# Performance work log

Hardware: AMD Instinct MI355X
Metric: run time of the kernel (lower is better)

Reference implementation:

```python
import jax, jax.numpy as jnp
import numpy as np

N_NODES = 100000
N_GRAPHS = 64


def gcn_conv(x, src, dst, W, b, num_nodes):
    """PyG GCNConv: add self-loops, symmetric deg normalization, aggregate at dst."""
    h = x @ W  # [N, out]
    ones_e = jnp.ones(src.shape[0], dtype=x.dtype)
    # degree includes self-loop (+1)
    deg = jax.ops.segment_sum(ones_e, dst, num_segments=num_nodes) + 1.0
    dinv = jnp.where(deg > 0, 1.0 / jnp.sqrt(deg), 0.0)  # deg>=1 always here
    norm = dinv[src] * dinv[dst]  # [E]
    msg = h[src] * norm[:, None]  # gather + scale
    agg = jax.ops.segment_sum(msg, dst, num_segments=num_nodes)
    # self-loop contribution: norm_ii = dinv[i]^2
    agg = agg + h * (dinv * dinv)[:, None]
    return agg + b


def global_mean_pool(x, batch, num_graphs):
    sums = jax.ops.segment_sum(x, batch, num_segments=num_graphs)
    counts = jax.ops.segment_sum(jnp.ones(x.shape[0], dtype=x.dtype), batch,
                                 num_segments=num_graphs)
    return sums / jnp.maximum(counts, 1.0)[:, None]


def setup_inputs() -> dict:
    key = jax.random.key(0)
    ks = jax.random.split(key, 8)
    H = 128
    x = jax.random.normal(ks[0], (N_NODES, 4), dtype=jnp.float32)
    edge_index = jax.random.randint(ks[1], (2, 1600000), 0, N_NODES, dtype=jnp.int64 if jax.config.read('jax_enable_x64') else jnp.int32)
    batch = jnp.sort(jax.random.randint(ks[2], (N_NODES,), 0, N_GRAPHS))
    def glorot(k, shape):
        fan_in, fan_out = shape
        lim = np.sqrt(6.0 / (fan_in + fan_out))
        return jax.random.uniform(k, shape, jnp.float32, -lim, lim)
    return {
        'x': x,
        'edge_index': edge_index,
        'batch': batch,
        'W1': glorot(ks[3], (4, H)), 'b1': jnp.zeros((H,), jnp.float32),
        'W2': glorot(ks[4], (H, H)), 'b2': jnp.zeros((H,), jnp.float32),
        'W3': glorot(ks[5], (H, H)), 'b3': jnp.zeros((H,), jnp.float32),
        'Wl': glorot(ks[6], (H, 2)), 'bl': jnp.zeros((2,), jnp.float32),
    }


def reference(x, edge_index, batch, W1, b1, W2, b2, W3, b3, Wl, bl):
    src, dst = edge_index[0], edge_index[1]
    h = jax.nn.relu(gcn_conv(x, src, dst, W1, b1, N_NODES))
    h = jax.nn.relu(gcn_conv(h, src, dst, W2, b2, N_NODES))
    h = jax.nn.relu(gcn_conv(h, src, dst, W3, b3, N_NODES))
    g = global_mean_pool(h, batch, N_GRAPHS)  # [G, H]
    logits = g @ Wl + bl  # [G, 2]
    return jax.nn.log_softmax(logits, axis=1)
```

## Files before the change

### kernel.cpp

```cpp
#include <hip/hip_runtime.h>

#define HDIM 128
#define NGRAPH 64

#define BSHIFT 9
#define NBUCK 196
#define BCAP 48
#define BSTR 49
#define RCAP 9216
#define BIN_CHUNK 4096

typedef __attribute__((ext_vector_type(8))) short short8;
typedef __attribute__((ext_vector_type(4))) float floatx4;
typedef __attribute__((ext_vector_type(2))) float floatx2;

__device__ __forceinline__ float bf2f(unsigned short u) {
    union { unsigned int i; float f; } v;
    v.i = ((unsigned int)u) << 16;
    return v.f;
}
__device__ __forceinline__ unsigned short f2bf(float f) {
    unsigned int u = __float_as_uint(f);
    u += 0x7FFFu + ((u >> 16) & 1u);
    return (unsigned short)(u >> 16);
}

__global__ __launch_bounds__(256) void k_misc(int* __restrict__ gcur,
                                              const int* __restrict__ batch,
                                              float* __restrict__ gcnt,
                                              float* __restrict__ gsum,
                                              const float* __restrict__ W2,
                                              unsigned short* __restrict__ Wp2,
                                              const float* __restrict__ W3,
                                              unsigned short* __restrict__ Wp3,
                                              int N, int nbuck) {
    int t = threadIdx.x;
    int blk = blockIdx.x;
    if (blk == 0) {
        if (t < nbuck) gcur[t] = t * RCAP;
        for (int i = t; i < NGRAPH * 128; i += 256) gsum[i] = 0.f;
        if (t < NGRAPH) {
            int g = t;
            int lo = 0, hi = N;
            while (lo < hi) { int m = (lo + hi) >> 1; if (batch[m] < g) lo = m + 1; else hi = m; }
            int lb = lo;
            lo = 0; hi = N;
            while (lo < hi) { int m = (lo + hi) >> 1; if (batch[m] < g + 1) lo = m + 1; else hi = m; }
            gcnt[g] = (float)(lo - lb);
        }
        return;
    }
    const float* W = (blk <= 64) ? W2 : W3;
    unsigned short* Wp = (blk <= 64) ? Wp2 : Wp3;
    int idx = ((blk <= 64) ? (blk - 1) : (blk - 65)) * 256 + t;
    int j = idx & 7, l = (idx >> 3) & 63, frag = idx >> 9;
    int c = frag >> 2, ks = frag & 3;
    int k = ks * 32 + ((l >> 4) & 3) * 8 + j;
    int n = c * 16 + (l & 15);
    Wp[idx] = f2bf(W[k * 128 + n]);
}


__global__ __launch_bounds__(256) void k_binA(const int* __restrict__ src,
                                              const int* __restrict__ dst,
                                              int* __restrict__ gcur,
                                              unsigned int* __restrict__ binned, int E) {
    __shared__ unsigned int bin[NBUCK * BSTR];
    __shared__ int bcnt[NBUCK];
    __shared__ int bbase[NBUCK];
    int t = threadIdx.x;
    for (int b = t; b < NBUCK; b += 256) bcnt[b] = 0;
    __syncthreads();
    int e0 = blockIdx.x * BIN_CHUNK;
    #pragma unroll
    for (int i = 0; i < BIN_CHUNK / 1024; i++) {
        int e = e0 + i * 1024 + t * 4;
        if (e + 3 < E) {
            const int4 d4 = *(const int4*)&dst[e];
            const int4 s4 = *(const int4*)&src[e];
            int dd[4] = {d4.x, d4.y, d4.z, d4.w};
            int ss[4] = {s4.x, s4.y, s4.z, s4.w};
            #pragma unroll
            for (int k = 0; k < 4; k++) {
                int d = dd[k];
                unsigned int rec = ((unsigned int)(d & 511) << 20) | (unsigned int)ss[k];
                int b = d >> BSHIFT;
                int idx = atomicAdd(&bcnt[b], 1);
                if (idx < BCAP) bin[b * BSTR + idx] = rec;
                else { int p = atomicAdd(&gcur[b], 1); binned[p] = rec; }
            }
        } else {
            for (int k = 0; k < 4; k++) {
                int e2 = e + k;
                if (e2 < E) {
                    int d = dst[e2];
                    unsigned int rec = ((unsigned int)(d & 511) << 20) | (unsigned int)src[e2];
                    int b = d >> BSHIFT;
                    int idx = atomicAdd(&bcnt[b], 1);
                    if (idx < BCAP) bin[b * BSTR + idx] = rec;
                    else { int p = atomicAdd(&gcur[b], 1); binned[p] = rec; }
                }
            }
        }
    }
    __syncthreads();
    if (t < NBUCK) {
        int cnt = min(bcnt[t], BCAP);
        bbase[t] = atomicAdd(&gcur[t], cnt);
    }
    __syncthreads();
    int wave = t >> 6, lane = t & 63;
    for (int b = wave; b < NBUCK; b += 4) {
        int cnt = min(bcnt[b], BCAP);
        int base = bbase[b];
        if (lane < cnt) binned[base + lane] = bin[b * BSTR + lane];
    }
}

__global__ __launch_bounds__(256) void k_fillB(const int* __restrict__ gcur,
                                               const unsigned int* __restrict__ binned,
                                               int* __restrict__ P,
                                               float* __restrict__ dinv,
                                               int* __restrict__ csr,
                                               const float4* __restrict__ x4,
                                               float4* __restrict__ xs4,
                                               int N, int nbuck) {
    __shared__ int ps[256];
    __shared__ int cnt[512];
    __shared__ int image[RCAP];
    int b = blockIdx.x;
    int t = threadIdx.x;
    int lt = (t < nbuck) ? (gcur[t] - t * RCAP) : 0;
    ps[t] = lt;
    __syncthreads();
    for (int d = 1; d < 256; d <<= 1) {
        int o = (t >= d) ? ps[t - d] : 0;
        __syncthreads();
        ps[t] += o;
        __syncthreads();
    }
    int start = (b > 0) ? ps[b - 1] : 0;
    int len = ps[b] - start;
    __syncthreads();

    int n0 = b << BSHIFT;
    int nloc = min(n0 + 512, N) - n0;
    cnt[t] = 0; cnt[t + 256] = 0;
    __syncthreads();
    const unsigned int* rb = binned + (size_t)b * RCAP;
    for (int i = t; i < len; i += 256) atomicAdd(&cnt[rb[i] >> 20], 1);
    __syncthreads();
    int c0 = cnt[2 * t], c1 = cnt[2 * t + 1];
    int pair = c0 + c1;
    __syncthreads();
    cnt[t] = pair;
    __syncthreads();
    for (int d = 1; d < 256; d <<= 1) {
        int o = (t >= d) ? cnt[t - d] : 0;
        __syncthreads();
        cnt[t] += o;
        __syncthreads();
    }
    int excl = cnt[t] - pair;
    __syncthreads();
    if (2 * t < nloc) {
        int n = n0 + 2 * t;
        float dv0 = rsqrtf((float)c0 + 1.0f);
        P[n] = start + excl;
        dinv[n] = dv0;
        float4 xv = x4[n];
        xs4[n] = make_float4(xv.x * dv0, xv.y * dv0, xv.z * dv0, xv.w * dv0);
    }
    if (2 * t + 1 < nloc) {
        int n = n0 + 2 * t + 1;
        float dv1 = rsqrtf((float)c1 + 1.0f);
        P[n] = start + excl + c0;
        dinv[n] = dv1;
        float4 xv = x4[n];
        xs4[n] = make_float4(xv.x * dv1, xv.y * dv1, xv.z * dv1, xv.w * dv1);
    }
    if (b == nbuck - 1 && t == 0) P[N] = start + len;
    cnt[2 * t] = excl;
    cnt[2 * t + 1] = excl + c0;
    __syncthreads();
    for (int i = t; i < len; i += 256) {
        unsigned int rec = rb[i];
        int pos = atomicAdd(&cnt[rec >> 20], 1);
        image[pos] = (int)(rec & 0xFFFFFu);
    }
    __syncthreads();
    for (int i = t; i < len; i += 256) csr[start + i] = image[i];
}

__global__ void k_aggx_csr(const int* __restrict__ P, const int* __restrict__ csr,
                           const float4* __restrict__ xs, const float* __restrict__ dinv,
                           float4* __restrict__ aggx, int N) {
    int d = blockIdx.x * blockDim.x + threadIdx.x;
    if (d >= N) return;
    int s0 = P[d], s1 = P[d + 1];
    float dd = dinv[d];
    float4 sv = xs[d];
    float4 a = make_float4(sv.x * dd, sv.y * dd, sv.z * dd, sv.w * dd);
    int i = s0;
    int pre = min(s1, (s0 + 3) & ~3);
    for (; i < pre; i++) {
        float4 v = xs[csr[i]];
        a.x += v.x; a.y += v.y; a.z += v.z; a.w += v.w;
    }
    for (; i + 8 <= s1; i += 8) {
        const int4 iA = *(const int4*)&csr[i];
        const int4 iB = *(const int4*)&csr[i + 4];
        float4 vA = xs[iA.x], vB = xs[iA.y], vC = xs[iA.z], vD = xs[iA.w];
        float4 vE = xs[iB.x], vF = xs[iB.y], vG = xs[iB.z], vH = xs[iB.w];
        a.x += vA.x + vB.x + vC.x + vD.x + vE.x + vF.x + vG.x + vH.x;
        a.y += vA.y + vB.y + vC.y + vD.y + vE.y + vF.y + vG.y + vH.y;
        a.z += vA.z + vB.z + vC.z + vD.z + vE.z + vF.z + vG.z + vH.z;
        a.w += vA.w + vB.w + vC.w + vD.w + vE.w + vF.w + vG.w + vH.w;
    }
    for (; i + 4 <= s1; i += 4) {
        const int4 ix = *(const int4*)&csr[i];
        float4 vA = xs[ix.x], vB = xs[ix.y], vC = xs[ix.z], vD = xs[ix.w];
        a.x += vA.x + vB.x + vC.x + vD.x;
        a.y += vA.y + vB.y + vC.y + vD.y;
        a.z += vA.z + vB.z + vC.z + vD.z;
        a.w += vA.w + vB.w + vC.w + vD.w;
    }
    for (; i < s1; i++) {
        float4 v = xs[csr[i]];
        a.x += v.x; a.y += v.y; a.z += v.z; a.w += v.w;
    }
    aggx[d] = make_float4(a.x * dd, a.y * dd, a.z * dd, a.w * dd);
}

#define LXS 136
__global__ __launch_bounds__(256) void k_l1t2(const float4* __restrict__ aggx,
                                              const float* __restrict__ W1,
                                              const float* __restrict__ b1,
                                              const unsigned short* __restrict__ Wp,
                                              const float* __restrict__ dinv,
                                              unsigned char* __restrict__ out8, int N) {
    __shared__ unsigned short lx[64 * LXS];
    __shared__ unsigned short lw[16384];
    __shared__ float w1s[512];
    __shared__ float b1s[128];
    __shared__ float ax[64][4];
    int t = threadIdx.x;
    int n0 = blockIdx.x * 64;

    for (int i = t; i < 512; i += 256) w1s[i] = W1[i];
    if (t < 128) b1s[t] = b1[t];
    if (t < 64) {
        float4 v = (n0 + t < N) ? aggx[n0 + t] : make_float4(0.f, 0.f, 0.f, 0.f);
        ax[t][0] = v.x; ax[t][1] = v.y; ax[t][2] = v.z; ax[t][3] = v.w;
    }
    for (int ch = t; ch < 2048; ch += 256)
        *(uint4*)&lw[ch * 8] = *(const uint4*)&Wp[ch * 8];
    __syncthreads();

    for (int i = t; i < 8192; i += 256) {
        int n = i >> 7, j = i & 127;
        float v = b1s[j] + ax[n][0] * w1s[j] + ax[n][1] * w1s[128 + j]
                         + ax[n][2] * w1s[256 + j] + ax[n][3] * w1s[384 + j];
        lx[n * LXS + j] = f2bf(fmaxf(v, 0.f));
    }
    __syncthreads();

    int w = t >> 6, lane = t & 63;
    int m0 = w * 16;
    int col = lane & 15, quad = lane >> 4;

    short8 afrag[4];
    #pragma unroll
    for (int ks = 0; ks < 4; ks++)
        afrag[ks] = *(const short8*)&lx[(m0 + col) * LXS + ks * 32 + quad * 8];

    float dv[4];
    #pragma unroll
    for (int r = 0; r < 4; r++) {
        int gn = n0 + m0 + quad * 4 + r;
        dv[r] = (gn < N) ? dinv[gn] : 0.0f;
    }

    #pragma unroll
    for (int c = 0; c < 8; c++) {
        floatx4 acc = {0.f, 0.f, 0.f, 0.f};
        #pragma unroll
        for (int ks = 0; ks < 4; ks++) {
            const short8 bfrag = *(const short8*)&lw[((c * 4 + ks) * 64 + lane) * 8];
            acc = __builtin_amdgcn_mfma_f32_16x16x32_bf16(afrag[ks], bfrag, acc, 0, 0, 0);
        }
        int j = c * 16 + col;
        size_t sbase = (size_t)(j >> 5) * N * 32 + (size_t)(j & 31);
        #pragma unroll
        for (int r = 0; r < 4; r++) {
            int gn = n0 + m0 + quad * 4 + r;
            if (gn < N) {
                float v = acc[r] * dv[r];
                out8[sbase + (size_t)gn * 32] =
                    (unsigned char)(__builtin_amdgcn_cvt_pk_fp8_f32(v, v, 0, false) & 0xFF);
            }
        }
    }
}

__global__ __launch_bounds__(256) void k_transform_mfma(const unsigned short* __restrict__ in,
                                                        const unsigned short* __restrict__ Wp,
                                                        const float* __restrict__ dinv,
                                                        unsigned char* __restrict__ out8, int N) {
    __shared__ unsigned short lx[64 * LXS];
    __shared__ unsigned short lw[16384];
    int t = threadIdx.x;
    int n0 = blockIdx.x * 64;

    for (int ch = t; ch < 1024; ch += 256) {
        int row = ch >> 4, part = ch & 15;
        uint4 val = make_uint4(0, 0, 0, 0);
        if (n0 + row < N) val = *(const uint4*)&in[(size_t)(n0 + row) * 128 + part * 8];
        *(uint4*)&lx[row * LXS + part * 8] = val;
    }
    for (int ch = t; ch < 2048; ch += 256)
        *(uint4*)&lw[ch * 8] = *(const uint4*)&Wp[ch * 8];
    __syncthreads();

    int w = t >> 6, lane = t & 63;
    int m0 = w * 16;
    int col = lane & 15, quad = lane >> 4;

    short8 afrag[4];
    #pragma unroll
    for (int ks = 0; ks < 4; ks++)
        afrag[ks] = *(const short8*)&lx[(m0 + col) * LXS + ks * 32 + quad * 8];

    float dv[4];
    #pragma unroll
    for (int r = 0; r < 4; r++) {
        int gn = n0 + m0 + quad * 4 + r;
        dv[r] = (gn < N) ? dinv[gn] : 0.0f;
    }

    #pragma unroll
    for (int c = 0; c < 8; c++) {
        floatx4 acc = {0.f, 0.f, 0.f, 0.f};
        #pragma unroll
        for (int ks = 0; ks < 4; ks++) {
            const short8 bfrag = *(const short8*)&lw[((c * 4 + ks) * 64 + lane) * 8];
            acc = __builtin_amdgcn_mfma_f32_16x16x32_bf16(afrag[ks], bfrag, acc, 0, 0, 0);
        }
        int j = c * 16 + col;
        size_t sbase = (size_t)(j >> 5) * N * 32 + (size_t)(j & 31);
        #pragma unroll
        for (int r = 0; r < 4; r++) {
            int gn = n0 + m0 + quad * 4 + r;
            if (gn < N) {
                float v = acc[r] * dv[r];
                out8[sbase + (size_t)gn * 32] =
                    (unsigned char)(__builtin_amdgcn_cvt_pk_fp8_f32(v, v, 0, false) & 0xFF);
            }
        }
    }
}

__device__ __forceinline__ void fp8acc(unsigned int u, float& a0, float& a1,
                                       float& a2, float& a3) {
    floatx2 lo = __builtin_amdgcn_cvt_pk_f32_fp8(u, false);
    floatx2 hi = __builtin_amdgcn_cvt_pk_f32_fp8(u, true);
    a0 += lo.x; a1 += lo.y; a2 += hi.x; a3 += hi.y;
}

__device__ __forceinline__ void gather8(const int* __restrict__ csr,
                                        const unsigned int* __restrict__ stab,
                                        int s0, int s1,
                                        float& a0, float& a1, float& a2, float& a3) {
    int i = s0;
    int pre = min(s1, (s0 + 3) & ~3);
    for (; i < pre; i++)
        fp8acc(stab[(size_t)csr[i] * 8], a0, a1, a2, a3);
    for (; i + 8 <= s1; i += 8) {
        const int4 iA = *(const int4*)&csr[i];
        const int4 iB = *(const int4*)&csr[i + 4];
        unsigned int u0 = stab[(size_t)iA.x * 8];
        unsigned int u1 = stab[(size_t)iA.y * 8];
        unsigned int u2 = stab[(size_t)iA.z * 8];
        unsigned int u3 = stab[(size_t)iA.w * 8];
        unsigned int u4 = stab[(size_t)iB.x * 8];
        unsigned int u5 = stab[(size_t)iB.y * 8];
        unsigned int u6 = stab[(size_t)iB.z * 8];
        unsigned int u7 = stab[(size_t)iB.w * 8];
        fp8acc(u0, a0, a1, a2, a3); fp8acc(u1, a0, a1, a2, a3);
        fp8acc(u2, a0, a1, a2, a3); fp8acc(u3, a0, a1, a2, a3);
        fp8acc(u4, a0, a1, a2, a3); fp8acc(u5, a0, a1, a2, a3);
        fp8acc(u6, a0, a1, a2, a3); fp8acc(u7, a0, a1, a2, a3);
    }
    for (; i + 4 <= s1; i += 4) {
        const int4 iA = *(const int4*)&csr[i];
        unsigned int u0 = stab[(size_t)iA.x * 8];
        unsigned int u1 = stab[(size_t)iA.y * 8];
        unsigned int u2 = stab[(size_t)iA.z * 8];
        unsigned int u3 = stab[(size_t)iA.w * 8];
        fp8acc(u0, a0, a1, a2, a3); fp8acc(u1, a0, a1, a2, a3);
        fp8acc(u2, a0, a1, a2, a3); fp8acc(u3, a0, a1, a2, a3);
    }
    for (; i < s1; i++)
        fp8acc(stab[(size_t)csr[i] * 8], a0, a1, a2, a3);
}

__global__ __launch_bounds__(256) void k_agg_sl(const int* __restrict__ P,
                                                const int* __restrict__ csr,
                                                const unsigned int* __restrict__ tab,
                                                const float* __restrict__ dinv,
                                                const float* __restrict__ bias,
                                                unsigned short* __restrict__ out16,
                                                const int* __restrict__ batch,
                                                float* __restrict__ gsum,
                                                int N, int mode) {
    __shared__ float psum[32][32];
    int t = threadIdx.x;
    int bid = blockIdx.x;
    int xcd = bid & 7;
    int slice = xcd >> 1;
    int chunk = (bid >> 3) * 2 + (xcd & 1);
    int nb = chunk * 32;
    int grp = t >> 3;
    int l = t & 7;
    int g = nb + grp;
    const unsigned int* stab = tab + (size_t)slice * N * 8 + l;

    float o0 = 0.f, o1 = 0.f, o2 = 0.f, o3 = 0.f;
    if (g < N) {
        int s0 = P[g], s1 = P[g + 1];
        unsigned int su = stab[(size_t)g * 8];
        floatx2 slo = __builtin_amdgcn_cvt_pk_f32_fp8(su, false);
        floatx2 shi = __builtin_amdgcn_cvt_pk_f32_fp8(su, true);
        float a0 = slo.x, a1 = slo.y, a2 = shi.x, a3 = shi.y;
        gather8(csr, stab, s0, s1, a0, a1, a2, a3);
        float dd = dinv[g];
        const float4 bb = *(const float4*)&bias[slice * 32 + l * 4];
        o0 = fmaxf(a0 * dd + bb.x, 0.f);
        o1 = fmaxf(a1 * dd + bb.y, 0.f);
        o2 = fmaxf(a2 * dd + bb.z, 0.f);
        o3 = fmaxf(a3 * dd + bb.w, 0.f);
        if (mode == 0) {
            ushort4 o;
            o.x = f2bf(o0); o.y = f2bf(o1); o.z = f2bf(o2); o.w = f2bf(o3);
            *(ushort4*)&out16[(size_t)g * 128 + slice * 32 + l * 4] = o;
        }
    }
    if (mode != 0) {
        *(float4*)&psum[grp][l * 4] = make_float4(o0, o1, o2, o3);
        __syncthreads();
        if (t < 32 && nb < N) {
            int f = t;
            int nbN = min(32, N - nb);
            int b0 = batch[nb], bL = batch[nb + nbN - 1];
            if (b0 == bL) {
                float s = 0.f;
                #pragma unroll
                for (int n = 0; n < 32; n++) s += psum[n][f];
                unsafeAtomicAdd(&gsum[(size_t)b0 * 128 + slice * 32 + f], s);
            } else {
                float acc = 0.f; int cur = b0;
                for (int n = 0; n < nbN; n++) {
                    int bb = batch[nb + n];
                    if (bb != cur) {
                        unsafeAtomicAdd(&gsum[(size_t)cur * 128 + slice * 32 + f], acc);
                        acc = 0.f; cur = bb;
                    }
                    acc += psum[n][f];
                }
                unsafeAtomicAdd(&gsum[(size_t)cur * 128 + slice * 32 + f], acc);
            }
        }
    }
}

__global__ __launch_bounds__(256) void k_head(const float* __restrict__ gsum,
                                              const float* __restrict__ gcnt,
                                              const float* __restrict__ Wl,
                                              const float* __restrict__ bl,
                                              float* __restrict__ out, int G) {
    int t = threadIdx.x;
    int g = t >> 2, q = t & 3;
    if (g >= G) return;
    float l0 = 0.f, l1 = 0.f;
    #pragma unroll
    for (int k = 0; k < 32; k++) {
        int jj = q * 32 + k;
        float v = gsum[(size_t)g * 128 + jj];
        l0 += v * Wl[jj * 2 + 0];
        l1 += v * Wl[jj * 2 + 1];
    }
    l0 += __shfl_xor(l0, 1, 64); l1 += __shfl_xor(l1, 1, 64);
    l0 += __shfl_xor(l0, 2, 64); l1 += __shfl_xor(l1, 2, 64);
    if (q == 0) {
        float inv = 1.0f / fmaxf(gcnt[g], 1.0f);
        l0 = l0 * inv + bl[0];
        l1 = l1 * inv + bl[1];
        float m = fmaxf(l0, l1);
        float lse = m + logf(expf(l0 - m) + expf(l1 - m));
        out[g * 2 + 0] = l0 - lse;
        out[g * 2 + 1] = l1 - lse;
    }
}


extern "C" void kernel_launch(void* const* d_in, const int* in_sizes, int n_in,
                              void* d_out, int out_size, void* d_ws, size_t ws_size,
                              hipStream_t stream) {
    const float* x   = (const float*)d_in[0];
    const int*   ei  = (const int*)d_in[1];
    const int*   bat = (const int*)d_in[2];
    const float* W1  = (const float*)d_in[3];
    const float* b1  = (const float*)d_in[4];
    const float* W2  = (const float*)d_in[5];
    const float* b2  = (const float*)d_in[6];
    const float* W3  = (const float*)d_in[7];
    const float* b3  = (const float*)d_in[8];
    const float* Wl  = (const float*)d_in[9];
    const float* bl  = (const float*)d_in[10];

    const int N = in_sizes[0] / 4;
    const int E = in_sizes[1] / 2;
    const int* srcI = ei;
    const int* dstI = ei + E;

    const int nbuck = (N + 511) >> BSHIFT;
    const int pAlloc = ((N + 1 + 3) & ~3) + 4;

    float* wsf  = (float*)d_ws;
    float* dinv = wsf;
    int*   P    = (int*)(dinv + N);
    int*   csr  = P + pAlloc;
    float* aggx = (float*)(csr + E);
    unsigned short* bufA16 = (unsigned short*)(aggx + (size_t)N * 4);
    unsigned char*  hs8    = (unsigned char*)(bufA16 + (size_t)N * 128);
    unsigned short* Wp2    = (unsigned short*)(hs8 + (size_t)N * 128);
    unsigned short* Wp3    = Wp2 + 16384;
    float* gsum = (float*)(Wp3 + 16384);
    float* gcnt = gsum + NGRAPH * 128;
    int*   gcur = (int*)(gcnt + NGRAPH);
    unsigned int* binned = (unsigned int*)hs8;
    float* xs4 = (float*)bufA16;

    const int chunks = (N + 31) >> 5;
    const int aggGrid = ((chunks + 1) >> 1) * 8;

    k_misc<<<129, 256, 0, stream>>>(gcur, bat, gcnt, gsum, W2, Wp2, W3, Wp3, N, nbuck);
    k_binA<<<(E + BIN_CHUNK - 1) / BIN_CHUNK, 256, 0, stream>>>(srcI, dstI, gcur, binned, E);
    k_fillB<<<nbuck, 256, 0, stream>>>(gcur, binned, P, dinv, csr,
                                       (const float4*)x, (float4*)xs4, N, nbuck);

    k_aggx_csr<<<(N + 255) / 256, 256, 0, stream>>>(P, csr, (const float4*)xs4, dinv,
                                                    (float4*)aggx, N);
    k_l1t2<<<(N + 63) / 64, 256, 0, stream>>>((const float4*)aggx, W1, b1, Wp2, dinv, hs8, N);

    k_agg_sl<<<aggGrid, 256, 0, stream>>>(P, csr, (const unsigned int*)hs8,
                                          dinv, b2, bufA16, nullptr, nullptr, N, 0);

    k_transform_mfma<<<(N + 63) / 64, 256, 0, stream>>>(bufA16, Wp3, dinv, hs8, N);
    k_agg_sl<<<aggGrid, 256, 0, stream>>>(P, csr, (const unsigned int*)hs8,
                                          dinv, b3, nullptr, bat, gsum, N, 1);

    k_head<<<1, 256, 0, stream>>>(gsum, gcnt, Wl, bl, (float*)d_out, NGRAPH);
}
```

Baseline: 305.1 us.

## Sort nodes by degree within aggregation blocks and use nontemporal stores

In the aggregation kernel, each block now ranks its 32 nodes by in-degree and assigns them to 8-lane groups in sorted order. Nodes with similar gather loop lengths then share a wavefront, which is meant to reduce divergence. Separately, several kernels now write outputs with nontemporal stores (binned records, CSR indices, aggx, fp8 tables, bf16 activations) to avoid cache pollution. The ranking adds two barriers and a small O(32) loop per block. Nontemporal stores may hurt when the data is re-read soon by the next kernel.

```diff
diff --git a/kernel.cpp b/kernel.cpp
--- a/kernel.cpp
+++ b/kernel.cpp
@@ -13,6 +13,7 @@
 typedef __attribute__((ext_vector_type(8))) short short8;
 typedef __attribute__((ext_vector_type(4))) float floatx4;
 typedef __attribute__((ext_vector_type(2))) float floatx2;
+typedef __attribute__((ext_vector_type(4))) unsigned short ushortx4;
 
 __device__ __forceinline__ float bf2f(unsigned short u) {
     union { unsigned int i; float f; } v;
@@ -24,6 +25,7 @@
     u += 0x7FFFu + ((u >> 16) & 1u);
     return (unsigned short)(u >> 16);
 }
+
 
 __global__ __launch_bounds__(256) void k_misc(int* __restrict__ gcur,
                                               const int* __restrict__ batch,
@@ -113,7 +115,7 @@
     for (int b = wave; b < NBUCK; b += 4) {
         int cnt = min(bcnt[b], BCAP);
         int base = bbase[b];
-        if (lane < cnt) binned[base + lane] = bin[b * BSTR + lane];
+        if (lane < cnt) __builtin_nontemporal_store(bin[b * BSTR + lane], &binned[base + lane]);
     }
 }
 
@@ -189,7 +191,8 @@
         image[pos] = (int)(rec & 0xFFFFFu);
     }
     __syncthreads();
-    for (int i = t; i < len; i += 256) csr[start + i] = image[i];
+    for (int i = t; i < len; i += 256)
+        __builtin_nontemporal_store(image[i], &csr[start + i]);
 }
 
 __global__ void k_aggx_csr(const int* __restrict__ P, const int* __restrict__ csr,
@@ -229,7 +232,8 @@
         float4 v = xs[csr[i]];
         a.x += v.x; a.y += v.y; a.z += v.z; a.w += v.w;
     }
-    aggx[d] = make_float4(a.x * dd, a.y * dd, a.z * dd, a.w * dd);
+    floatx4 o = {a.x * dd, a.y * dd, a.z * dd, a.w * dd};
+    __builtin_nontemporal_store(o, (floatx4*)&aggx[d]);
 }
 
 #define LXS 136
@@ -296,8 +300,9 @@
             int gn = n0 + m0 + quad * 4 + r;
             if (gn < N) {
                 float v = acc[r] * dv[r];
-                out8[sbase + (size_t)gn * 32] =
+                unsigned char pv =
                     (unsigned char)(__builtin_amdgcn_cvt_pk_fp8_f32(v, v, 0, false) & 0xFF);
+                __builtin_nontemporal_store(pv, &out8[sbase + (size_t)gn * 32]);
             }
         }
     }
@@ -353,8 +358,9 @@
             int gn = n0 + m0 + quad * 4 + r;
             if (gn < N) {
                 float v = acc[r] * dv[r];
-                out8[sbase + (size_t)gn * 32] =
+                unsigned char pv =
                     (unsigned char)(__builtin_amdgcn_cvt_pk_fp8_f32(v, v, 0, false) & 0xFF);
+                __builtin_nontemporal_store(pv, &out8[sbase + (size_t)gn * 32]);
             }
         }
     }
@@ -414,15 +420,36 @@
                                                 float* __restrict__ gsum,
                                                 int N, int mode) {
     __shared__ float psum[32][32];
+    __shared__ int sord[32];
     int t = threadIdx.x;
     int bid = blockIdx.x;
     int xcd = bid & 7;
     int slice = xcd >> 1;
     int chunk = (bid >> 3) * 2 + (xcd & 1);
     int nb = chunk * 32;
+
+    int* sdeg = (int*)psum;
+    if (t < 32) {
+        int gg = nb + t;
+        sdeg[t] = (gg < N) ? (P[gg + 1] - P[gg]) : -1;
+    }
+    __syncthreads();
+    if (t < 32) {
+        int dg = sdeg[t];
+        int rank = 0;
+        #pragma unroll
+        for (int j = 0; j < 32; j++) {
+            int dj = sdeg[j];
+            rank += (dj < dg) || (dj == dg && j < t);
+        }
+        sord[rank] = t;
+    }
+    __syncthreads();
+
     int grp = t >> 3;
     int l = t & 7;
-    int g = nb + grp;
+    int local = sord[grp];
+    int g = nb + local;
     const unsigned int* stab = tab + (size_t)slice * N * 8 + l;
 
     float o0 = 0.f, o1 = 0.f, o2 = 0.f, o3 = 0.f;
@@ -440,13 +467,14 @@
         o2 = fmaxf(a2 * dd + bb.z, 0.f);
         o3 = fmaxf(a3 * dd + bb.w, 0.f);
         if (mode == 0) {
-            ushort4 o;
-            o.x = f2bf(o0); o.y = f2bf(o1); o.z = f2bf(o2); o.w = f2bf(o3);
-            *(ushort4*)&out16[(size_t)g * 128 + slice * 32 + l * 4] = o;
+            ushortx4 o = {f2bf(o0), f2bf(o1), f2bf(o2), f2bf(o3)};
+            __builtin_nontemporal_store(
+                o, (ushortx4*)&out16[(size_t)g * 128 + slice * 32 + l * 4]);
         }
     }
     if (mode != 0) {
-        *(float4*)&psum[grp][l * 4] = make_float4(o0, o1, o2, o3);
+        __syncthreads();
+        *(float4*)&psum[local][l * 4] = make_float4(o0, o1, o2, o3);
         __syncthreads();
         if (t < 32 && nb < N) {
             int f = t;
```

After: 334.8 us. +9.7%, slower.

## Split neighbor gather across lane slots with 16-byte fp8 loads and shuffle reduction

Applied to the files above, without the earlier changes.

The aggregation kernel previously had each of 8 lanes per node load 4 bytes of fp8 features for every neighbor. Now the 8 lanes form 4 edge slots times 2 halves: each lane loads 16 bytes per neighbor for a quarter of the edges, and partial sums are reduced with xor shuffles. The goal is wider memory transactions and fewer gather instructions. In exchange each lane holds 16 accumulators, adds shuffle work, and leaves more lanes idle on low-degree tails. Output stores now use nontemporal 16-byte writes.

```diff
diff --git a/kernel.cpp b/kernel.cpp
--- a/kernel.cpp
+++ b/kernel.cpp
@@ -13,6 +13,7 @@
 typedef __attribute__((ext_vector_type(8))) short short8;
 typedef __attribute__((ext_vector_type(4))) float floatx4;
 typedef __attribute__((ext_vector_type(2))) float floatx2;
+typedef __attribute__((ext_vector_type(4))) unsigned int uintx4;
 
 __device__ __forceinline__ float bf2f(unsigned short u) {
     union { unsigned int i; float f; } v;
@@ -24,6 +25,7 @@
     u += 0x7FFFu + ((u >> 16) & 1u);
     return (unsigned short)(u >> 16);
 }
+
 
 __global__ __launch_bounds__(256) void k_misc(int* __restrict__ gcur,
                                               const int* __restrict__ batch,
@@ -360,48 +362,16 @@
     }
 }
 
-__device__ __forceinline__ void fp8acc(unsigned int u, float& a0, float& a1,
-                                       float& a2, float& a3) {
-    floatx2 lo = __builtin_amdgcn_cvt_pk_f32_fp8(u, false);
-    floatx2 hi = __builtin_amdgcn_cvt_pk_f32_fp8(u, true);
-    a0 += lo.x; a1 += lo.y; a2 += hi.x; a3 += hi.y;
-}
-
-__device__ __forceinline__ void gather8(const int* __restrict__ csr,
-                                        const unsigned int* __restrict__ stab,
-                                        int s0, int s1,
-                                        float& a0, float& a1, float& a2, float& a3) {
-    int i = s0;
-    int pre = min(s1, (s0 + 3) & ~3);
-    for (; i < pre; i++)
-        fp8acc(stab[(size_t)csr[i] * 8], a0, a1, a2, a3);
-    for (; i + 8 <= s1; i += 8) {
-        const int4 iA = *(const int4*)&csr[i];
-        const int4 iB = *(const int4*)&csr[i + 4];
-        unsigned int u0 = stab[(size_t)iA.x * 8];
-        unsigned int u1 = stab[(size_t)iA.y * 8];
-        unsigned int u2 = stab[(size_t)iA.z * 8];
-        unsigned int u3 = stab[(size_t)iA.w * 8];
-        unsigned int u4 = stab[(size_t)iB.x * 8];
-        unsigned int u5 = stab[(size_t)iB.y * 8];
-        unsigned int u6 = stab[(size_t)iB.z * 8];
-        unsigned int u7 = stab[(size_t)iB.w * 8];
-        fp8acc(u0, a0, a1, a2, a3); fp8acc(u1, a0, a1, a2, a3);
-        fp8acc(u2, a0, a1, a2, a3); fp8acc(u3, a0, a1, a2, a3);
-        fp8acc(u4, a0, a1, a2, a3); fp8acc(u5, a0, a1, a2, a3);
-        fp8acc(u6, a0, a1, a2, a3); fp8acc(u7, a0, a1, a2, a3);
-    }
-    for (; i + 4 <= s1; i += 4) {
-        const int4 iA = *(const int4*)&csr[i];
-        unsigned int u0 = stab[(size_t)iA.x * 8];
-        unsigned int u1 = stab[(size_t)iA.y * 8];
-        unsigned int u2 = stab[(size_t)iA.z * 8];
-        unsigned int u3 = stab[(size_t)iA.w * 8];
-        fp8acc(u0, a0, a1, a2, a3); fp8acc(u1, a0, a1, a2, a3);
-        fp8acc(u2, a0, a1, a2, a3); fp8acc(u3, a0, a1, a2, a3);
-    }
-    for (; i < s1; i++)
-        fp8acc(stab[(size_t)csr[i] * 8], a0, a1, a2, a3);
+__device__ __forceinline__ void dec16(uint4 u, float* a) {
+    floatx2 p;
+    p = __builtin_amdgcn_cvt_pk_f32_fp8(u.x, false); a[0] += p.x; a[1] += p.y;
+    p = __builtin_amdgcn_cvt_pk_f32_fp8(u.x, true);  a[2] += p.x; a[3] += p.y;
+    p = __builtin_amdgcn_cvt_pk_f32_fp8(u.y, false); a[4] += p.x; a[5] += p.y;
+    p = __builtin_amdgcn_cvt_pk_f32_fp8(u.y, true);  a[6] += p.x; a[7] += p.y;
+    p = __builtin_amdgcn_cvt_pk_f32_fp8(u.z, false); a[8] += p.x; a[9] += p.y;
+    p = __builtin_amdgcn_cvt_pk_f32_fp8(u.z, true);  a[10] += p.x; a[11] += p.y;
+    p = __builtin_amdgcn_cvt_pk_f32_fp8(u.w, false); a[12] += p.x; a[13] += p.y;
+    p = __builtin_amdgcn_cvt_pk_f32_fp8(u.w, true);  a[14] += p.x; a[15] += p.y;
 }
 
 __global__ __launch_bounds__(256) void k_agg_sl(const int* __restrict__ P,
@@ -421,32 +391,99 @@
     int chunk = (bid >> 3) * 2 + (xcd & 1);
     int nb = chunk * 32;
     int grp = t >> 3;
-    int l = t & 7;
+    int lg = t & 7;
+    int slot = lg >> 1;
+    int half = lg & 1;
     int g = nb + grp;
-    const unsigned int* stab = tab + (size_t)slice * N * 8 + l;
-
-    float o0 = 0.f, o1 = 0.f, o2 = 0.f, o3 = 0.f;
+    const unsigned int* sl = tab + (size_t)slice * N * 8;
+    int hofs = half * 4;
+
+    float a[16];
+    #pragma unroll
+    for (int j = 0; j < 16; j++) a[j] = 0.f;
+
     if (g < N) {
         int s0 = P[g], s1 = P[g + 1];
-        unsigned int su = stab[(size_t)g * 8];
-        floatx2 slo = __builtin_amdgcn_cvt_pk_f32_fp8(su, false);
-        floatx2 shi = __builtin_amdgcn_cvt_pk_f32_fp8(su, true);
-        float a0 = slo.x, a1 = slo.y, a2 = shi.x, a3 = shi.y;
-        gather8(csr, stab, s0, s1, a0, a1, a2, a3);
+        int i = s0;
+        int a0 = min(s1, (s0 + 3) & ~3);
+        if (i < a0) {
+            int k = i + slot;
+            if (k < a0) {
+                int e = csr[k];
+                uint4 u = *(const uint4*)&sl[(size_t)e * 8 + hofs];
+                dec16(u, a);
+            }
+            i = a0;
+        }
+        for (; i + 8 <= s1; i += 8) {
+            const int4 iv0 = *(const int4*)&csr[i];
+            const int4 iv1 = *(const int4*)&csr[i + 4];
+            int e0 = (slot & 1) ? ((slot & 2) ? iv0.w : iv0.y)
+                                : ((slot & 2) ? iv0.z : iv0.x);
+            int e1 = (slot & 1) ? ((slot & 2) ? iv1.w : iv1.y)
+                                : ((slot & 2) ? iv1.z : iv1.x);
+            uint4 u0 = *(const uint4*)&sl[(size_t)e0 * 8 + hofs];
+            uint4 u1 = *(const uint4*)&sl[(size_t)e1 * 8 + hofs];
+            dec16(u0, a);
+            dec16(u1, a);
+        }
+        for (; i + 4 <= s1; i += 4) {
+            const int4 iv = *(const int4*)&csr[i];
+            int e = (slot & 1) ? ((slot & 2) ? iv.w : iv.y)
+                               : ((slot & 2) ? iv.z : iv.x);
+            uint4 u = *(const uint4*)&sl[(size_t)e * 8 + hofs];
+            dec16(u, a);
+        }
+        if (i < s1) {
+            int k = i + slot;
+            if (k < s1) {
+                int e = csr[k];
+                uint4 u = *(const uint4*)&sl[(size_t)e * 8 + hofs];
+                dec16(u, a);
+            }
+        }
+        if (slot == 0) {
+            uint4 su = *(const uint4*)&sl[(size_t)g * 8 + hofs];
+            dec16(su, a);
+        }
+    }
+
+    #pragma unroll
+    for (int j = 0; j < 16; j++) {
+        a[j] += __shfl_xor(a[j], 2);
+        a[j] += __shfl_xor(a[j], 4);
+    }
+
+    float o[16];
+    #pragma unroll
+    for (int j = 0; j < 16; j++) o[j] = 0.f;
+    if (g < N) {
         float dd = dinv[g];
-        const float4 bb = *(const float4*)&bias[slice * 32 + l * 4];
-        o0 = fmaxf(a0 * dd + bb.x, 0.f);
-        o1 = fmaxf(a1 * dd + bb.y, 0.f);
-        o2 = fmaxf(a2 * dd + bb.z, 0.f);
-        o3 = fmaxf(a3 * dd + bb.w, 0.f);
-        if (mode == 0) {
-            ushort4 o;
-            o.x = f2bf(o0); o.y = f2bf(o1); o.z = f2bf(o2); o.w = f2bf(o3);
-            *(ushort4*)&out16[(size_t)g * 128 + slice * 32 + l * 4] = o;
+        const float* bb = &bias[slice * 32 + half * 16];
+        #pragma unroll
+        for (int j = 0; j < 16; j++) o[j] = fmaxf(a[j] * dd + bb[j], 0.f);
+        if (mode == 0 && slot == 0) {
+            uintx4 w0, w1;
+            w0.x = (unsigned int)f2bf(o[0]) | ((unsigned int)f2bf(o[1]) << 16);
+            w0.y = (unsigned int)f2bf(o[2]) | ((unsigned int)f2bf(o[3]) << 16);
+            w0.z = (unsigned int)f2bf(o[4]) | ((unsigned int)f2bf(o[5]) << 16);
+            w0.w = (unsigned int)f2bf(o[6]) | ((unsigned int)f2bf(o[7]) << 16);
+            w1.x = (unsigned int)f2bf(o[8]) | ((unsigned int)f2bf(o[9]) << 16);
+            w1.y = (unsigned int)f2bf(o[10]) | ((unsigned int)f2bf(o[11]) << 16);
+            w1.z = (unsigned int)f2bf(o[12]) | ((unsigned int)f2bf(o[13]) << 16);
+            w1.w = (unsigned int)f2bf(o[14]) | ((unsigned int)f2bf(o[15]) << 16);
+            unsigned short* dst = &out16[(size_t)g * 128 + slice * 32 + half * 16];
+            __builtin_nontemporal_store(w0, (uintx4*)dst);
+            __builtin_nontemporal_store(w1, (uintx4*)(dst + 8));
         }
     }
     if (mode != 0) {
-        *(float4*)&psum[grp][l * 4] = make_float4(o0, o1, o2, o3);
+        if (slot == 0) {
+            #pragma unroll
+            for (int q = 0; q < 4; q++)
+                *(float4*)&psum[grp][half * 16 + q * 4] =
+                    make_float4(o[q * 4], o[q * 4 + 1], o[q * 4 + 2], o[q * 4 + 3]);
+        }
         __syncthreads();
         if (t < 32 && nb < N) {
             int f = t;
```

Result: slower. 315.8 us (+3.5%).
